# Performance work log

Measured on AMD Instinct MI355X. Metric: run time of the kernel, lower is better.

The kernel has to match this reference:

```python
import jax, jax.numpy as jnp
import numpy as np

T = 8  # number of DP iterations (self.T)

def setup_inputs() -> dict:
    key = jax.random.key(0)
    ks = jax.random.split(key, 9)
    bs, dims, L, d = 16, 4, 2048, 256
    x = jax.random.uniform(ks[0], (bs, dims, L), dtype=jnp.float32)  # one-hot-like input
    s_in = 1.0 / np.sqrt(dims)
    s_d = 1.0 / np.sqrt(d)
    W1 = jax.random.uniform(ks[1], (d, dims), minval=-s_in, maxval=s_in, dtype=jnp.float32)
    b1 = jax.random.uniform(ks[2], (d,), minval=-s_in, maxval=s_in, dtype=jnp.float32)
    W2 = jax.random.uniform(ks[3], (d, d), minval=-s_d, maxval=s_d, dtype=jnp.float32)
    b2 = jax.random.uniform(ks[4], (d,), minval=-s_d, maxval=s_d, dtype=jnp.float32)
    W3 = jax.random.uniform(ks[5], (d, dims), minval=-s_in, maxval=s_in, dtype=jnp.float32)
    b3 = jax.random.uniform(ks[6], (d,), minval=-s_in, maxval=s_in, dtype=jnp.float32)
    W4 = jax.random.uniform(ks[7], (d, d), minval=-s_d, maxval=s_d, dtype=jnp.float32)
    b4 = jax.random.uniform(ks[8], (d,), minval=-s_d, maxval=s_d, dtype=jnp.float32)
    return dict(x=x, W1=W1, b1=b1, W2=W2, b2=b2, W3=W3, b3=b3, W4=W4, b4=b4)

def reference(x, W1, b1, W2, b2, W3, b3, W4, b4):
    # x: (bs, dims, L). The original allocates V:(bs,T+1,L+2,L+2,d) but only the
    # two diagonals V[i,j,j+1] ("up") and V[i,j,j-1] ("down") are ever written/read,
    # so the recurrence collapses to two (bs,L,d) lanes.
    a = jnp.einsum('bdl,od->blo', x, W1) + b1  # W1(x_j) for all j: (bs, L, d)
    bs, L, d = a.shape
    zcol = jnp.zeros((bs, 1, d), a.dtype)
    shift_r = lambda v: jnp.concatenate([zcol, v[:, :-1]], axis=1)  # v[j-1], zero at j=0
    shift_l = lambda v: jnp.concatenate([v[:, 1:], zcol], axis=1)   # v[j+1], zero at j=L-1
    up = jnp.zeros_like(a)   # up[j]   = V[i, j+1, j+2] (0-indexed lane)
    down = jnp.zeros_like(a) # down[j] = V[i, j+1, j]
    for _ in range(T):
        up = jax.nn.relu(a + shift_r(up) @ W2.T + b2)
        down = jax.nn.relu(a + shift_l(down) @ W2.T + b2)
    c = jnp.einsum('bdl,od->blo', x, W3) + b3
    # miu[j] = relu(W3 x_j + W4(V[T,j-1,j]) + W4(V[T,j+1,j]))
    miu = jax.nn.relu(c + (shift_r(up) @ W4.T + b4) + (shift_l(down) @ W4.T + b4))
    return miu  # (bs, L, d)
```

## Files before the change

### kernel.cpp

```cpp
#include <hip/hip_runtime.h>


typedef __bf16 bf16x8 __attribute__((ext_vector_type(8)));
typedef float f32x16 __attribute__((ext_vector_type(16)));

#define MFMA32(a, b, c) __builtin_amdgcn_mfma_f32_32x32x16_bf16(a, b, c, 0, 0, 0)

__device__ __forceinline__ unsigned short f2bf(float f) {
  unsigned int u = __builtin_bit_cast(unsigned int, f);
  u += 0x7fffu + ((u >> 16) & 1u);
  return (unsigned short)(u >> 16);
}
__device__ __forceinline__ float bf2f(unsigned short s) {
  unsigned int u = ((unsigned int)s) << 16;
  return __builtin_bit_cast(float, u);
}

__global__ void prep_kernel(const float* __restrict__ W1, const float* __restrict__ b1,
                            const float* __restrict__ W2, const float* __restrict__ b2,
                            const float* __restrict__ W3, const float* __restrict__ b3,
                            const float* __restrict__ W4, const float* __restrict__ b4,
                            unsigned short* __restrict__ ws) {
  int idx = blockIdx.x * 256 + threadIdx.x;
  if (idx >= 139264) return;
  float v = 0.0f;
  if (idx < 131072) {
    const float* W = (idx < 65536) ? W2 : W4;
    int i = idx & 65535;
    int j = i & 7, f = i >> 3;
    int lane = f & 63, slot = f >> 6;
    int ks = slot & 15, ot = slot >> 4;
    int o = ot * 32 + (lane & 31);
    int k = ks * 16 + (lane >> 5) * 8 + j;
    v = W[o * 256 + k];
  } else {
    int i = idx - 131072;
    bool first = (i < 4096);
    int ii = i & 4095;
    int j = ii & 7, f = ii >> 3;
    int lane = f & 63, ot = f >> 6;
    int o = ot * 32 + (lane & 31);
    if (lane < 32) {
      if (j < 4) v = first ? W1[o * 4 + j] : W3[o * 4 + j];
      else if (j == 4) v = first ? (b1[o] + b2[o]) : (b3[o] + 2.0f * b4[o]);
    }
  }
  ws[idx] = f2bf(v);
}

__global__ __launch_bounds__(256, 2)
void chain_kernel(const float* __restrict__ x, const unsigned short* __restrict__ ws,
                  float* __restrict__ out) {
  __shared__ int4 Ubuf[2][64 * 32];
  __shared__ int4 xw[80];
  __shared__ int4 zc;

  const int tid = threadIdx.x;
  const int l = tid & 63;
  const int w = tid >> 6;
  const int lane31 = l & 31;
  const int khalf = l >> 5;
  const int b = blockIdx.x >> 5;
  const int j0 = (blockIdx.x & 31) * 64;

  const int4* w2f = (const int4*)ws;
  const int4* w4f = (const int4*)(ws + 65536);
  const int4* w1xg = (const int4*)(ws + 131072);
  const int4* w3xg = (const int4*)(ws + 135168);

  if (tid == 0) zc = make_int4(0, 0, 0, 0);
  if (tid < 80) {
    int j = j0 - 8 + tid;
    int4 c = make_int4(0, 0, 0, 0);
    if (j >= 0 && j < 2048) {
      const float* xb = x + (b * 4) * 2048 + j;
      unsigned short h0 = f2bf(xb[0]);
      unsigned short h1 = f2bf(xb[2048]);
      unsigned short h2 = f2bf(xb[4096]);
      unsigned short h3 = f2bf(xb[6144]);
      c = make_int4((int)(h0 | ((unsigned int)h1 << 16)),
                    (int)(h2 | ((unsigned int)h3 << 16)),
                    0x00003f80, 0);
    }
    xw[tid] = c;
  }

  const int ot0 = w * 2;
  bf16x8 w2c[2][8];
  bf16x8 w1x[2];
#pragma unroll
  for (int t2 = 0; t2 < 2; ++t2) {
    w1x[t2] = __builtin_bit_cast(bf16x8, w1xg[(ot0 + t2) * 64 + l]);
#pragma unroll
    for (int ks = 0; ks < 8; ++ks)
      w2c[t2][ks] = __builtin_bit_cast(bf16x8, w2f[((ot0 + t2) * 16 + ks) * 64 + l]);
  }
  __syncthreads();

  const int mrow0 = lane31;
  const int mrow1 = 32 + lane31;

#pragma unroll 1
  for (int phase = 0; phase < 2; ++phase) {
    int4* U = Ubuf[phase];
#pragma unroll 1
    for (int t = 1; t <= 8; ++t) {
      f32x16 acc[2][2] = {};
#pragma unroll
      for (int mt = 0; mt < 2; ++mt) {
        int m = mt ? mrow1 : mrow0;
        int widx = (phase == 0) ? (m + t - 1) : (m + 17 - t);
        const int4* p = (l < 32) ? (xw + widx) : (&zc);
        bf16x8 bx = __builtin_bit_cast(bf16x8, *p);
        acc[mt][0] = MFMA32(w1x[0], bx, acc[mt][0]);
        acc[mt][1] = MFMA32(w1x[1], bx, acc[mt][1]);
      }
      if (t > 1) {
#pragma unroll
        for (int ks = 0; ks < 16; ++ks) {
          int c0 = 2 * ks + khalf;
          bf16x8 bu0 = __builtin_bit_cast(bf16x8, U[mrow0 * 32 + (c0 ^ (mrow0 & 7))]);
          bf16x8 bu1 = __builtin_bit_cast(bf16x8, U[mrow1 * 32 + (c0 ^ (mrow1 & 7))]);
          bf16x8 af0, af1;
          if (ks < 8) { af0 = w2c[0][ks]; af1 = w2c[1][ks]; }
          else {
            af0 = __builtin_bit_cast(bf16x8, w2f[(ot0 * 16 + ks) * 64 + l]);
            af1 = __builtin_bit_cast(bf16x8, w2f[((ot0 + 1) * 16 + ks) * 64 + l]);
          }
          acc[0][0] = MFMA32(af0, bu0, acc[0][0]);
          acc[0][1] = MFMA32(af1, bu0, acc[0][1]);
          acc[1][0] = MFMA32(af0, bu1, acc[1][0]);
          acc[1][1] = MFMA32(af1, bu1, acc[1][1]);
        }
      }
      __syncthreads();
      const bool lastdown = (phase == 1) && (t == 8);
#pragma unroll
      for (int mt = 0; mt < 2; ++mt) {
        int row = mt ? mrow1 : mrow0;
#pragma unroll
        for (int t2 = 0; t2 < 2; ++t2) {
          int ot = ot0 + t2;
#pragma unroll
          for (int q = 0; q < 4; ++q) {
            float v0 = fmaxf(acc[mt][t2][4 * q + 0], 0.0f);
            float v1 = fmaxf(acc[mt][t2][4 * q + 1], 0.0f);
            float v2 = fmaxf(acc[mt][t2][4 * q + 2], 0.0f);
            float v3 = fmaxf(acc[mt][t2][4 * q + 3], 0.0f);
            int co = ot * 4 + q;
            int coff = row * 32 + (co ^ (row & 7));
            if (lastdown) {
              uint2 uv = *(const uint2*)((const char*)(Ubuf[0] + coff) + khalf * 8);
              v0 += bf2f((unsigned short)(uv.x & 0xffffu));
              v1 += bf2f((unsigned short)(uv.x >> 16));
              v2 += bf2f((unsigned short)(uv.y & 0xffffu));
              v3 += bf2f((unsigned short)(uv.y >> 16));
            }
            uint2 pk;
            pk.x = f2bf(v0) | ((unsigned int)f2bf(v1) << 16);
            pk.y = f2bf(v2) | ((unsigned int)f2bf(v3) << 16);
            *(uint2*)((char*)(U + coff) + khalf * 8) = pk;
          }
        }
      }
      __syncthreads();
    }
  }

  {
    f32x16 acc[2][2] = {};
    bf16x8 w3x0 = __builtin_bit_cast(bf16x8, w3xg[ot0 * 64 + l]);
    bf16x8 w3x1 = __builtin_bit_cast(bf16x8, w3xg[(ot0 + 1) * 64 + l]);
#pragma unroll
    for (int mt = 0; mt < 2; ++mt) {
      int m = mt ? mrow1 : mrow0;
      const int4* p = (l < 32) ? (xw + (m + 8)) : (&zc);
      bf16x8 bx = __builtin_bit_cast(bf16x8, *p);
      acc[mt][0] = MFMA32(w3x0, bx, acc[mt][0]);
      acc[mt][1] = MFMA32(w3x1, bx, acc[mt][1]);
    }
    const int4* S = Ubuf[1];
#pragma unroll
    for (int ks = 0; ks < 16; ++ks) {
      int c0 = 2 * ks + khalf;
      bf16x8 bu0 = __builtin_bit_cast(bf16x8, S[mrow0 * 32 + (c0 ^ (mrow0 & 7))]);
      bf16x8 bu1 = __builtin_bit_cast(bf16x8, S[mrow1 * 32 + (c0 ^ (mrow1 & 7))]);
      bf16x8 af0 = __builtin_bit_cast(bf16x8, w4f[(ot0 * 16 + ks) * 64 + l]);
      bf16x8 af1 = __builtin_bit_cast(bf16x8, w4f[((ot0 + 1) * 16 + ks) * 64 + l]);
      acc[0][0] = MFMA32(af0, bu0, acc[0][0]);
      acc[0][1] = MFMA32(af1, bu0, acc[0][1]);
      acc[1][0] = MFMA32(af0, bu1, acc[1][0]);
      acc[1][1] = MFMA32(af1, bu1, acc[1][1]);
    }
#pragma unroll
    for (int mt = 0; mt < 2; ++mt) {
      int m = mt ? mrow1 : mrow0;
      int pbase = (b * 2048 + j0 + m) * 256;
#pragma unroll
      for (int t2 = 0; t2 < 2; ++t2) {
#pragma unroll
        for (int q = 0; q < 4; ++q) {
          int ob = (ot0 + t2) * 32 + 8 * q + 4 * khalf;
          float4 v;
          v.x = fmaxf(acc[mt][t2][4 * q + 0], 0.0f);
          v.y = fmaxf(acc[mt][t2][4 * q + 1], 0.0f);
          v.z = fmaxf(acc[mt][t2][4 * q + 2], 0.0f);
          v.w = fmaxf(acc[mt][t2][4 * q + 3], 0.0f);
          *(float4*)(out + pbase + ob) = v;
        }
      }
    }
  }
}

extern "C" void kernel_launch(void* const* d_in, const int* in_sizes, int n_in,
                              void* d_out, int out_size, void* d_ws, size_t ws_size,
                              hipStream_t stream) {
  const float* x  = (const float*)d_in[0];
  const float* W1 = (const float*)d_in[1];
  const float* b1 = (const float*)d_in[2];
  const float* W2 = (const float*)d_in[3];
  const float* b2 = (const float*)d_in[4];
  const float* W3 = (const float*)d_in[5];
  const float* b3 = (const float*)d_in[6];
  const float* W4 = (const float*)d_in[7];
  const float* b4 = (const float*)d_in[8];
  unsigned short* ws = (unsigned short*)d_ws;

  prep_kernel<<<544, 256, 0, stream>>>(W1, b1, W2, b2, W3, b3, W4, b4, ws);
  chain_kernel<<<512, 256, 0, stream>>>(x, ws, (float*)d_out);
}
```

Baseline: 159.6 us.

## Run up and down recurrence phases concurrently in separate wave groups

Doubles the block to 512 threads so waves 0-3 compute the 'up' recurrence and waves 4-7 the 'down' recurrence at the same time, instead of running the two phases one after the other. The final W4 GEMM is split by row halves across the two wave groups, which accumulate over both U buffers instead of pre-summing them into one. Fewer W2 fragments are cached in registers to fit the 512-thread launch bound. Native bf16 conversions replace the manual packing. The risks are more register pressure and extra global loads of W2.

After: 273.7 us. 71.5% more time.

```diff
diff --git a/kernel.cpp b/kernel.cpp
--- a/kernel.cpp
+++ b/kernel.cpp
@@ -2,6 +2,7 @@
 
 
 typedef __bf16 bf16x8 __attribute__((ext_vector_type(8)));
+typedef __bf16 bf16x4 __attribute__((ext_vector_type(4)));
 typedef float f32x16 __attribute__((ext_vector_type(16)));
 
 #define MFMA32(a, b, c) __builtin_amdgcn_mfma_f32_32x32x16_bf16(a, b, c, 0, 0, 0)
@@ -10,10 +11,6 @@
   unsigned int u = __builtin_bit_cast(unsigned int, f);
   u += 0x7fffu + ((u >> 16) & 1u);
   return (unsigned short)(u >> 16);
-}
-__device__ __forceinline__ float bf2f(unsigned short s) {
-  unsigned int u = ((unsigned int)s) << 16;
-  return __builtin_bit_cast(float, u);
 }
 
 __global__ void prep_kernel(const float* __restrict__ W1, const float* __restrict__ b1,
@@ -48,7 +45,7 @@
   ws[idx] = f2bf(v);
 }
 
-__global__ __launch_bounds__(256, 2)
+__global__ __launch_bounds__(512, 4)
 void chain_kernel(const float* __restrict__ x, const unsigned short* __restrict__ ws,
                   float* __restrict__ out) {
   __shared__ int4 Ubuf[2][64 * 32];
@@ -58,6 +55,8 @@
   const int tid = threadIdx.x;
   const int l = tid & 63;
   const int w = tid >> 6;
+  const int phase = w >> 2;
+  const int ot0 = (w & 3) * 2;
   const int lane31 = l & 31;
   const int khalf = l >> 5;
   const int b = blockIdx.x >> 5;
@@ -85,129 +84,110 @@
     xw[tid] = c;
   }
 
-  const int ot0 = w * 2;
-  bf16x8 w2c[2][8];
+  bf16x8 w2c[2][4];
   bf16x8 w1x[2];
 #pragma unroll
   for (int t2 = 0; t2 < 2; ++t2) {
     w1x[t2] = __builtin_bit_cast(bf16x8, w1xg[(ot0 + t2) * 64 + l]);
 #pragma unroll
-    for (int ks = 0; ks < 8; ++ks)
+    for (int ks = 0; ks < 4; ++ks)
       w2c[t2][ks] = __builtin_bit_cast(bf16x8, w2f[((ot0 + t2) * 16 + ks) * 64 + l]);
   }
   __syncthreads();
 
   const int mrow0 = lane31;
   const int mrow1 = 32 + lane31;
+  int4* U = Ubuf[phase];
 
 #pragma unroll 1
-  for (int phase = 0; phase < 2; ++phase) {
-    int4* U = Ubuf[phase];
-#pragma unroll 1
-    for (int t = 1; t <= 8; ++t) {
-      f32x16 acc[2][2] = {};
-#pragma unroll
-      for (int mt = 0; mt < 2; ++mt) {
-        int m = mt ? mrow1 : mrow0;
-        int widx = (phase == 0) ? (m + t - 1) : (m + 17 - t);
-        const int4* p = (l < 32) ? (xw + widx) : (&zc);
-        bf16x8 bx = __builtin_bit_cast(bf16x8, *p);
-        acc[mt][0] = MFMA32(w1x[0], bx, acc[mt][0]);
-        acc[mt][1] = MFMA32(w1x[1], bx, acc[mt][1]);
-      }
-      if (t > 1) {
-#pragma unroll
-        for (int ks = 0; ks < 16; ++ks) {
-          int c0 = 2 * ks + khalf;
-          bf16x8 bu0 = __builtin_bit_cast(bf16x8, U[mrow0 * 32 + (c0 ^ (mrow0 & 7))]);
-          bf16x8 bu1 = __builtin_bit_cast(bf16x8, U[mrow1 * 32 + (c0 ^ (mrow1 & 7))]);
-          bf16x8 af0, af1;
-          if (ks < 8) { af0 = w2c[0][ks]; af1 = w2c[1][ks]; }
-          else {
-            af0 = __builtin_bit_cast(bf16x8, w2f[(ot0 * 16 + ks) * 64 + l]);
-            af1 = __builtin_bit_cast(bf16x8, w2f[((ot0 + 1) * 16 + ks) * 64 + l]);
-          }
-          acc[0][0] = MFMA32(af0, bu0, acc[0][0]);
-          acc[0][1] = MFMA32(af1, bu0, acc[0][1]);
-          acc[1][0] = MFMA32(af0, bu1, acc[1][0]);
-          acc[1][1] = MFMA32(af1, bu1, acc[1][1]);
+  for (int t = 1; t <= 8; ++t) {
+    f32x16 acc[2][2] = {};
+#pragma unroll
+    for (int mt = 0; mt < 2; ++mt) {
+      int m = mt ? mrow1 : mrow0;
+      int widx = (phase == 0) ? (m + t - 1) : (m + 17 - t);
+      const int4* p = (l < 32) ? (xw + widx) : (&zc);
+      bf16x8 bx = __builtin_bit_cast(bf16x8, *p);
+      acc[mt][0] = MFMA32(w1x[0], bx, acc[mt][0]);
+      acc[mt][1] = MFMA32(w1x[1], bx, acc[mt][1]);
+    }
+    if (t > 1) {
+#pragma unroll
+      for (int ks = 0; ks < 16; ++ks) {
+        int c0 = 2 * ks + khalf;
+        bf16x8 bu0 = __builtin_bit_cast(bf16x8, U[mrow0 * 32 + (c0 ^ (mrow0 & 7))]);
+        bf16x8 bu1 = __builtin_bit_cast(bf16x8, U[mrow1 * 32 + (c0 ^ (mrow1 & 7))]);
+        bf16x8 af0, af1;
+        if (ks < 4) { af0 = w2c[0][ks]; af1 = w2c[1][ks]; }
+        else {
+          af0 = __builtin_bit_cast(bf16x8, w2f[(ot0 * 16 + ks) * 64 + l]);
+          af1 = __builtin_bit_cast(bf16x8, w2f[((ot0 + 1) * 16 + ks) * 64 + l]);
         }
-      }
-      __syncthreads();
-      const bool lastdown = (phase == 1) && (t == 8);
-#pragma unroll
-      for (int mt = 0; mt < 2; ++mt) {
-        int row = mt ? mrow1 : mrow0;
-#pragma unroll
-        for (int t2 = 0; t2 < 2; ++t2) {
-          int ot = ot0 + t2;
-#pragma unroll
-          for (int q = 0; q < 4; ++q) {
-            float v0 = fmaxf(acc[mt][t2][4 * q + 0], 0.0f);
-            float v1 = fmaxf(acc[mt][t2][4 * q + 1], 0.0f);
-            float v2 = fmaxf(acc[mt][t2][4 * q + 2], 0.0f);
-            float v3 = fmaxf(acc[mt][t2][4 * q + 3], 0.0f);
-            int co = ot * 4 + q;
-            int coff = row * 32 + (co ^ (row & 7));
-            if (lastdown) {
-              uint2 uv = *(const uint2*)((const char*)(Ubuf[0] + coff) + khalf * 8);
-              v0 += bf2f((unsigned short)(uv.x & 0xffffu));
-              v1 += bf2f((unsigned short)(uv.x >> 16));
-              v2 += bf2f((unsigned short)(uv.y & 0xffffu));
-              v3 += bf2f((unsigned short)(uv.y >> 16));
-            }
-            uint2 pk;
-            pk.x = f2bf(v0) | ((unsigned int)f2bf(v1) << 16);
-            pk.y = f2bf(v2) | ((unsigned int)f2bf(v3) << 16);
-            *(uint2*)((char*)(U + coff) + khalf * 8) = pk;
-          }
+        acc[0][0] = MFMA32(af0, bu0, acc[0][0]);
+        acc[0][1] = MFMA32(af1, bu0, acc[0][1]);
+        acc[1][0] = MFMA32(af0, bu1, acc[1][0]);
+        acc[1][1] = MFMA32(af1, bu1, acc[1][1]);
+      }
+    }
+    __syncthreads();
+#pragma unroll
+    for (int mt = 0; mt < 2; ++mt) {
+      int row = mt ? mrow1 : mrow0;
+#pragma unroll
+      for (int t2 = 0; t2 < 2; ++t2) {
+        int ot = ot0 + t2;
+#pragma unroll
+        for (int q = 0; q < 4; ++q) {
+          bf16x4 h;
+          h.x = (__bf16)fmaxf(acc[mt][t2][4 * q + 0], 0.0f);
+          h.y = (__bf16)fmaxf(acc[mt][t2][4 * q + 1], 0.0f);
+          h.z = (__bf16)fmaxf(acc[mt][t2][4 * q + 2], 0.0f);
+          h.w = (__bf16)fmaxf(acc[mt][t2][4 * q + 3], 0.0f);
+          int co = ot * 4 + q;
+          int coff = row * 32 + (co ^ (row & 7));
+          *(uint2*)((char*)(U + coff) + khalf * 8) = __builtin_bit_cast(uint2, h);
         }
       }
-      __syncthreads();
-    }
+    }
+    __syncthreads();
   }
 
   {
-    f32x16 acc[2][2] = {};
+    const int mrow = phase * 32 + lane31;
+    f32x16 acc[2] = {};
     bf16x8 w3x0 = __builtin_bit_cast(bf16x8, w3xg[ot0 * 64 + l]);
     bf16x8 w3x1 = __builtin_bit_cast(bf16x8, w3xg[(ot0 + 1) * 64 + l]);
-#pragma unroll
-    for (int mt = 0; mt < 2; ++mt) {
-      int m = mt ? mrow1 : mrow0;
-      const int4* p = (l < 32) ? (xw + (m + 8)) : (&zc);
+    {
+      const int4* p = (l < 32) ? (xw + mrow + 8) : (&zc);
       bf16x8 bx = __builtin_bit_cast(bf16x8, *p);
-      acc[mt][0] = MFMA32(w3x0, bx, acc[mt][0]);
-      acc[mt][1] = MFMA32(w3x1, bx, acc[mt][1]);
-    }
-    const int4* S = Ubuf[1];
-#pragma unroll
-    for (int ks = 0; ks < 16; ++ks) {
-      int c0 = 2 * ks + khalf;
-      bf16x8 bu0 = __builtin_bit_cast(bf16x8, S[mrow0 * 32 + (c0 ^ (mrow0 & 7))]);
-      bf16x8 bu1 = __builtin_bit_cast(bf16x8, S[mrow1 * 32 + (c0 ^ (mrow1 & 7))]);
-      bf16x8 af0 = __builtin_bit_cast(bf16x8, w4f[(ot0 * 16 + ks) * 64 + l]);
-      bf16x8 af1 = __builtin_bit_cast(bf16x8, w4f[((ot0 + 1) * 16 + ks) * 64 + l]);
-      acc[0][0] = MFMA32(af0, bu0, acc[0][0]);
-      acc[0][1] = MFMA32(af1, bu0, acc[0][1]);
-      acc[1][0] = MFMA32(af0, bu1, acc[1][0]);
-      acc[1][1] = MFMA32(af1, bu1, acc[1][1]);
-    }
-#pragma unroll
-    for (int mt = 0; mt < 2; ++mt) {
-      int m = mt ? mrow1 : mrow0;
-      int pbase = (b * 2048 + j0 + m) * 256;
-#pragma unroll
-      for (int t2 = 0; t2 < 2; ++t2) {
-#pragma unroll
-        for (int q = 0; q < 4; ++q) {
-          int ob = (ot0 + t2) * 32 + 8 * q + 4 * khalf;
-          float4 v;
-          v.x = fmaxf(acc[mt][t2][4 * q + 0], 0.0f);
-          v.y = fmaxf(acc[mt][t2][4 * q + 1], 0.0f);
-          v.z = fmaxf(acc[mt][t2][4 * q + 2], 0.0f);
-          v.w = fmaxf(acc[mt][t2][4 * q + 3], 0.0f);
-          *(float4*)(out + pbase + ob) = v;
-        }
+      acc[0] = MFMA32(w3x0, bx, acc[0]);
+      acc[1] = MFMA32(w3x1, bx, acc[1]);
+    }
+#pragma unroll 1
+    for (int ph2 = 0; ph2 < 2; ++ph2) {
+      const int4* S = Ubuf[ph2];
+#pragma unroll
+      for (int ks = 0; ks < 16; ++ks) {
+        int c0 = 2 * ks + khalf;
+        bf16x8 bu = __builtin_bit_cast(bf16x8, S[mrow * 32 + (c0 ^ (mrow & 7))]);
+        bf16x8 af0 = __builtin_bit_cast(bf16x8, w4f[(ot0 * 16 + ks) * 64 + l]);
+        bf16x8 af1 = __builtin_bit_cast(bf16x8, w4f[((ot0 + 1) * 16 + ks) * 64 + l]);
+        acc[0] = MFMA32(af0, bu, acc[0]);
+        acc[1] = MFMA32(af1, bu, acc[1]);
+      }
+    }
+    int pbase = (b * 2048 + j0 + mrow) * 256;
+#pragma unroll
+    for (int t2 = 0; t2 < 2; ++t2) {
+#pragma unroll
+      for (int q = 0; q < 4; ++q) {
+        int ob = (ot0 + t2) * 32 + 8 * q + 4 * khalf;
+        float4 v;
+        v.x = fmaxf(acc[t2][4 * q + 0], 0.0f);
+        v.y = fmaxf(acc[t2][4 * q + 1], 0.0f);
+        v.z = fmaxf(acc[t2][4 * q + 2], 0.0f);
+        v.w = fmaxf(acc[t2][4 * q + 3], 0.0f);
+        *(float4*)(out + pbase + ob) = v;
       }
     }
   }
@@ -228,5 +208,5 @@
   unsigned short* ws = (unsigned short*)d_ws;
 
   prep_kernel<<<544, 256, 0, stream>>>(W1, b1, W2, b2, W3, b3, W4, b4, ws);
-  chain_kernel<<<512, 256, 0, stream>>>(x, ws, (float*)d_out);
-}
+  chain_kernel<<<512, 512, 0, stream>>>(x, ws, (float*)d_out);
+}
```

## Split up/down recurrence phases into separate blocks and add a final W4 kernel

Applied to the files above, without the earlier changes.

The up and down recurrences now run in separate thread blocks (1024 blocks instead of 512), each using a single 32 KB LDS state buffer with a launch bound of 4 blocks per CU. Each block writes its final state to global workspace, and a new final_kernel reloads both states and computes the W3/W4 output. This doubles parallelism and occupancy for the serial 8-step chain. The cost is an extra kernel launch and a global round-trip of the state tiles. The bf16 packing also switches to native __bf16 conversion, and the down state is no longer pre-summed with up before the W4 GEMM; instead two K-passes accumulate, which is more MFMA work in the final stage.

Measured after the change: 254.5 us. +59.5%, slower.

```diff
diff --git a/kernel.cpp b/kernel.cpp
--- a/kernel.cpp
+++ b/kernel.cpp
@@ -2,6 +2,7 @@
 
 
 typedef __bf16 bf16x8 __attribute__((ext_vector_type(8)));
+typedef __bf16 bf16x4 __attribute__((ext_vector_type(4)));
 typedef float f32x16 __attribute__((ext_vector_type(16)));
 
 #define MFMA32(a, b, c) __builtin_amdgcn_mfma_f32_32x32x16_bf16(a, b, c, 0, 0, 0)
@@ -11,10 +12,8 @@
   u += 0x7fffu + ((u >> 16) & 1u);
   return (unsigned short)(u >> 16);
 }
-__device__ __forceinline__ float bf2f(unsigned short s) {
-  unsigned int u = ((unsigned int)s) << 16;
-  return __builtin_bit_cast(float, u);
-}
+
+#define STATE_OFF 139264
 
 __global__ void prep_kernel(const float* __restrict__ W1, const float* __restrict__ b1,
                             const float* __restrict__ W2, const float* __restrict__ b2,
@@ -48,10 +47,9 @@
   ws[idx] = f2bf(v);
 }
 
-__global__ __launch_bounds__(256, 2)
-void chain_kernel(const float* __restrict__ x, const unsigned short* __restrict__ ws,
-                  float* __restrict__ out) {
-  __shared__ int4 Ubuf[2][64 * 32];
+__global__ __launch_bounds__(256, 4)
+void chain_kernel(const float* __restrict__ x, unsigned short* __restrict__ ws) {
+  __shared__ int4 U[64 * 32];
   __shared__ int4 xw[80];
   __shared__ int4 zc;
 
@@ -60,13 +58,13 @@
   const int w = tid >> 6;
   const int lane31 = l & 31;
   const int khalf = l >> 5;
-  const int b = blockIdx.x >> 5;
-  const int j0 = (blockIdx.x & 31) * 64;
+  const int phase = blockIdx.x >> 9;
+  const int tile = blockIdx.x & 511;
+  const int b = tile >> 5;
+  const int j0 = (tile & 31) * 64;
 
   const int4* w2f = (const int4*)ws;
-  const int4* w4f = (const int4*)(ws + 65536);
   const int4* w1xg = (const int4*)(ws + 131072);
-  const int4* w3xg = (const int4*)(ws + 135168);
 
   if (tid == 0) zc = make_int4(0, 0, 0, 0);
   if (tid < 80) {
@@ -101,90 +99,125 @@
   const int mrow1 = 32 + lane31;
 
 #pragma unroll 1
-  for (int phase = 0; phase < 2; ++phase) {
-    int4* U = Ubuf[phase];
-#pragma unroll 1
-    for (int t = 1; t <= 8; ++t) {
-      f32x16 acc[2][2] = {};
-#pragma unroll
-      for (int mt = 0; mt < 2; ++mt) {
-        int m = mt ? mrow1 : mrow0;
-        int widx = (phase == 0) ? (m + t - 1) : (m + 17 - t);
-        const int4* p = (l < 32) ? (xw + widx) : (&zc);
-        bf16x8 bx = __builtin_bit_cast(bf16x8, *p);
-        acc[mt][0] = MFMA32(w1x[0], bx, acc[mt][0]);
-        acc[mt][1] = MFMA32(w1x[1], bx, acc[mt][1]);
+  for (int t = 1; t <= 8; ++t) {
+    f32x16 acc[2][2] = {};
+#pragma unroll
+    for (int mt = 0; mt < 2; ++mt) {
+      int m = mt ? mrow1 : mrow0;
+      int widx = (phase == 0) ? (m + t - 1) : (m + 17 - t);
+      const int4* p = (l < 32) ? (xw + widx) : (&zc);
+      bf16x8 bx = __builtin_bit_cast(bf16x8, *p);
+      acc[mt][0] = MFMA32(w1x[0], bx, acc[mt][0]);
+      acc[mt][1] = MFMA32(w1x[1], bx, acc[mt][1]);
+    }
+    if (t > 1) {
+#pragma unroll
+      for (int ks = 0; ks < 16; ++ks) {
+        int c0 = 2 * ks + khalf;
+        bf16x8 bu0 = __builtin_bit_cast(bf16x8, U[mrow0 * 32 + (c0 ^ (mrow0 & 7))]);
+        bf16x8 bu1 = __builtin_bit_cast(bf16x8, U[mrow1 * 32 + (c0 ^ (mrow1 & 7))]);
+        bf16x8 af0, af1;
+        if (ks < 8) { af0 = w2c[0][ks]; af1 = w2c[1][ks]; }
+        else {
+          af0 = __builtin_bit_cast(bf16x8, w2f[(ot0 * 16 + ks) * 64 + l]);
+          af1 = __builtin_bit_cast(bf16x8, w2f[((ot0 + 1) * 16 + ks) * 64 + l]);
+        }
+        acc[0][0] = MFMA32(af0, bu0, acc[0][0]);
+        acc[0][1] = MFMA32(af1, bu0, acc[0][1]);
+        acc[1][0] = MFMA32(af0, bu1, acc[1][0]);
+        acc[1][1] = MFMA32(af1, bu1, acc[1][1]);
       }
-      if (t > 1) {
-#pragma unroll
-        for (int ks = 0; ks < 16; ++ks) {
-          int c0 = 2 * ks + khalf;
-          bf16x8 bu0 = __builtin_bit_cast(bf16x8, U[mrow0 * 32 + (c0 ^ (mrow0 & 7))]);
-          bf16x8 bu1 = __builtin_bit_cast(bf16x8, U[mrow1 * 32 + (c0 ^ (mrow1 & 7))]);
-          bf16x8 af0, af1;
-          if (ks < 8) { af0 = w2c[0][ks]; af1 = w2c[1][ks]; }
-          else {
-            af0 = __builtin_bit_cast(bf16x8, w2f[(ot0 * 16 + ks) * 64 + l]);
-            af1 = __builtin_bit_cast(bf16x8, w2f[((ot0 + 1) * 16 + ks) * 64 + l]);
-          }
-          acc[0][0] = MFMA32(af0, bu0, acc[0][0]);
-          acc[0][1] = MFMA32(af1, bu0, acc[0][1]);
-          acc[1][0] = MFMA32(af0, bu1, acc[1][0]);
-          acc[1][1] = MFMA32(af1, bu1, acc[1][1]);
+    }
+    __syncthreads();
+#pragma unroll
+    for (int mt = 0; mt < 2; ++mt) {
+      int row = mt ? mrow1 : mrow0;
+#pragma unroll
+      for (int t2 = 0; t2 < 2; ++t2) {
+        int ot = ot0 + t2;
+#pragma unroll
+        for (int q = 0; q < 4; ++q) {
+          bf16x4 h;
+          h.x = (__bf16)fmaxf(acc[mt][t2][4 * q + 0], 0.0f);
+          h.y = (__bf16)fmaxf(acc[mt][t2][4 * q + 1], 0.0f);
+          h.z = (__bf16)fmaxf(acc[mt][t2][4 * q + 2], 0.0f);
+          h.w = (__bf16)fmaxf(acc[mt][t2][4 * q + 3], 0.0f);
+          int co = ot * 4 + q;
+          int coff = row * 32 + (co ^ (row & 7));
+          *(uint2*)((char*)(U + coff) + khalf * 8) = __builtin_bit_cast(uint2, h);
         }
       }
-      __syncthreads();
-      const bool lastdown = (phase == 1) && (t == 8);
-#pragma unroll
-      for (int mt = 0; mt < 2; ++mt) {
-        int row = mt ? mrow1 : mrow0;
-#pragma unroll
-        for (int t2 = 0; t2 < 2; ++t2) {
-          int ot = ot0 + t2;
-#pragma unroll
-          for (int q = 0; q < 4; ++q) {
-            float v0 = fmaxf(acc[mt][t2][4 * q + 0], 0.0f);
-            float v1 = fmaxf(acc[mt][t2][4 * q + 1], 0.0f);
-            float v2 = fmaxf(acc[mt][t2][4 * q + 2], 0.0f);
-            float v3 = fmaxf(acc[mt][t2][4 * q + 3], 0.0f);
-            int co = ot * 4 + q;
-            int coff = row * 32 + (co ^ (row & 7));
-            if (lastdown) {
-              uint2 uv = *(const uint2*)((const char*)(Ubuf[0] + coff) + khalf * 8);
-              v0 += bf2f((unsigned short)(uv.x & 0xffffu));
-              v1 += bf2f((unsigned short)(uv.x >> 16));
-              v2 += bf2f((unsigned short)(uv.y & 0xffffu));
-              v3 += bf2f((unsigned short)(uv.y >> 16));
-            }
-            uint2 pk;
-            pk.x = f2bf(v0) | ((unsigned int)f2bf(v1) << 16);
-            pk.y = f2bf(v2) | ((unsigned int)f2bf(v3) << 16);
-            *(uint2*)((char*)(U + coff) + khalf * 8) = pk;
-          }
-        }
-      }
-      __syncthreads();
-    }
-  }
-
-  {
-    f32x16 acc[2][2] = {};
-    bf16x8 w3x0 = __builtin_bit_cast(bf16x8, w3xg[ot0 * 64 + l]);
-    bf16x8 w3x1 = __builtin_bit_cast(bf16x8, w3xg[(ot0 + 1) * 64 + l]);
-#pragma unroll
-    for (int mt = 0; mt < 2; ++mt) {
-      int m = mt ? mrow1 : mrow0;
-      const int4* p = (l < 32) ? (xw + (m + 8)) : (&zc);
-      bf16x8 bx = __builtin_bit_cast(bf16x8, *p);
-      acc[mt][0] = MFMA32(w3x0, bx, acc[mt][0]);
-      acc[mt][1] = MFMA32(w3x1, bx, acc[mt][1]);
-    }
-    const int4* S = Ubuf[1];
+    }
+    __syncthreads();
+  }
+
+  int4* stg = (int4*)(ws + STATE_OFF) + (phase * 512 + tile) * 2048;
+#pragma unroll
+  for (int i = 0; i < 8; ++i) stg[i * 256 + tid] = U[i * 256 + tid];
+}
+
+__global__ __launch_bounds__(256, 2)
+void final_kernel(const float* __restrict__ x, const unsigned short* __restrict__ ws,
+                  float* __restrict__ out) {
+  __shared__ int4 S[2][64 * 32];
+  __shared__ int4 xw[64];
+  __shared__ int4 zc;
+
+  const int tid = threadIdx.x;
+  const int l = tid & 63;
+  const int w = tid >> 6;
+  const int lane31 = l & 31;
+  const int khalf = l >> 5;
+  const int tile = blockIdx.x;
+  const int b = tile >> 5;
+  const int j0 = (tile & 31) * 64;
+
+  const int4* w4f = (const int4*)(ws + 65536);
+  const int4* w3xg = (const int4*)(ws + 135168);
+  const int4* stg = (const int4*)(ws + STATE_OFF);
+
+  if (tid == 0) zc = make_int4(0, 0, 0, 0);
+  if (tid < 64) {
+    int j = j0 + tid;
+    const float* xb = x + (b * 4) * 2048 + j;
+    unsigned short h0 = f2bf(xb[0]);
+    unsigned short h1 = f2bf(xb[2048]);
+    unsigned short h2 = f2bf(xb[4096]);
+    unsigned short h3 = f2bf(xb[6144]);
+    xw[tid] = make_int4((int)(h0 | ((unsigned int)h1 << 16)),
+                        (int)(h2 | ((unsigned int)h3 << 16)),
+                        0x00003f80, 0);
+  }
+#pragma unroll
+  for (int i = 0; i < 8; ++i) {
+    S[0][i * 256 + tid] = stg[tile * 2048 + i * 256 + tid];
+    S[1][i * 256 + tid] = stg[(512 + tile) * 2048 + i * 256 + tid];
+  }
+  __syncthreads();
+
+  const int ot0 = w * 2;
+  const int mrow0 = lane31;
+  const int mrow1 = 32 + lane31;
+
+  f32x16 acc[2][2] = {};
+  bf16x8 w3x0 = __builtin_bit_cast(bf16x8, w3xg[ot0 * 64 + l]);
+  bf16x8 w3x1 = __builtin_bit_cast(bf16x8, w3xg[(ot0 + 1) * 64 + l]);
+#pragma unroll
+  for (int mt = 0; mt < 2; ++mt) {
+    int m = mt ? mrow1 : mrow0;
+    const int4* p = (l < 32) ? (xw + m) : (&zc);
+    bf16x8 bx = __builtin_bit_cast(bf16x8, *p);
+    acc[mt][0] = MFMA32(w3x0, bx, acc[mt][0]);
+    acc[mt][1] = MFMA32(w3x1, bx, acc[mt][1]);
+  }
+#pragma unroll 1
+  for (int ph = 0; ph < 2; ++ph) {
+    const int4* Sp = S[ph];
 #pragma unroll
     for (int ks = 0; ks < 16; ++ks) {
       int c0 = 2 * ks + khalf;
-      bf16x8 bu0 = __builtin_bit_cast(bf16x8, S[mrow0 * 32 + (c0 ^ (mrow0 & 7))]);
-      bf16x8 bu1 = __builtin_bit_cast(bf16x8, S[mrow1 * 32 + (c0 ^ (mrow1 & 7))]);
+      bf16x8 bu0 = __builtin_bit_cast(bf16x8, Sp[mrow0 * 32 + (c0 ^ (mrow0 & 7))]);
+      bf16x8 bu1 = __builtin_bit_cast(bf16x8, Sp[mrow1 * 32 + (c0 ^ (mrow1 & 7))]);
       bf16x8 af0 = __builtin_bit_cast(bf16x8, w4f[(ot0 * 16 + ks) * 64 + l]);
       bf16x8 af1 = __builtin_bit_cast(bf16x8, w4f[((ot0 + 1) * 16 + ks) * 64 + l]);
       acc[0][0] = MFMA32(af0, bu0, acc[0][0]);
@@ -192,22 +225,22 @@
       acc[1][0] = MFMA32(af0, bu1, acc[1][0]);
       acc[1][1] = MFMA32(af1, bu1, acc[1][1]);
     }
-#pragma unroll
-    for (int mt = 0; mt < 2; ++mt) {
-      int m = mt ? mrow1 : mrow0;
-      int pbase = (b * 2048 + j0 + m) * 256;
-#pragma unroll
-      for (int t2 = 0; t2 < 2; ++t2) {
-#pragma unroll
-        for (int q = 0; q < 4; ++q) {
-          int ob = (ot0 + t2) * 32 + 8 * q + 4 * khalf;
-          float4 v;
-          v.x = fmaxf(acc[mt][t2][4 * q + 0], 0.0f);
-          v.y = fmaxf(acc[mt][t2][4 * q + 1], 0.0f);
-          v.z = fmaxf(acc[mt][t2][4 * q + 2], 0.0f);
-          v.w = fmaxf(acc[mt][t2][4 * q + 3], 0.0f);
-          *(float4*)(out + pbase + ob) = v;
-        }
+  }
+#pragma unroll
+  for (int mt = 0; mt < 2; ++mt) {
+    int m = mt ? mrow1 : mrow0;
+    int pbase = (b * 2048 + j0 + m) * 256;
+#pragma unroll
+    for (int t2 = 0; t2 < 2; ++t2) {
+#pragma unroll
+      for (int q = 0; q < 4; ++q) {
+        int ob = (ot0 + t2) * 32 + 8 * q + 4 * khalf;
+        float4 v;
+        v.x = fmaxf(acc[mt][t2][4 * q + 0], 0.0f);
+        v.y = fmaxf(acc[mt][t2][4 * q + 1], 0.0f);
+        v.z = fmaxf(acc[mt][t2][4 * q + 2], 0.0f);
+        v.w = fmaxf(acc[mt][t2][4 * q + 3], 0.0f);
+        *(float4*)(out + pbase + ob) = v;
       }
     }
   }
@@ -228,5 +261,6 @@
   unsigned short* ws = (unsigned short*)d_ws;
 
   prep_kernel<<<544, 256, 0, stream>>>(W1, b1, W2, b2, W3, b3, W4, b4, ws);
-  chain_kernel<<<512, 256, 0, stream>>>(x, ws, (float*)d_out);
-}
+  chain_kernel<<<1024, 256, 0, stream>>>(x, ws);
+  final_kernel<<<512, 256, 0, stream>>>(x, ws, (float*)d_out);
+}
```

## Interleave up and down recurrences in one loop with column-major LDS layout

Applied to the files above, without the earlier changes.

The two DP chains (up and down) now advance together inside a single 8-step loop, each step issuing MFMAs for both lanes. This halves the number of block barriers and gives the scheduler twice as many independent MFMAs per step to hide latency. The shared buffer moves from a swizzled row layout to a column-major [chunk][row] layout, and the final W4 projection runs separately over both buffers instead of summing them in bf16 first. In exchange the accumulator state doubles (more VGPRs), so the number of register-cached W2 chunks drops from 8 to 6, which adds global reloads.

Result: faster. 135.1 us (-15.4%).

```diff
diff --git a/kernel.cpp b/kernel.cpp
--- a/kernel.cpp
+++ b/kernel.cpp
@@ -2,6 +2,7 @@
 
 
 typedef __bf16 bf16x8 __attribute__((ext_vector_type(8)));
+typedef __bf16 bf16x4 __attribute__((ext_vector_type(4)));
 typedef float f32x16 __attribute__((ext_vector_type(16)));
 
 #define MFMA32(a, b, c) __builtin_amdgcn_mfma_f32_32x32x16_bf16(a, b, c, 0, 0, 0)
@@ -10,10 +11,6 @@
   unsigned int u = __builtin_bit_cast(unsigned int, f);
   u += 0x7fffu + ((u >> 16) & 1u);
   return (unsigned short)(u >> 16);
-}
-__device__ __forceinline__ float bf2f(unsigned short s) {
-  unsigned int u = ((unsigned int)s) << 16;
-  return __builtin_bit_cast(float, u);
 }
 
 __global__ void prep_kernel(const float* __restrict__ W1, const float* __restrict__ b1,
@@ -48,10 +45,12 @@
   ws[idx] = f2bf(v);
 }
 
+#define NC 6
+
 __global__ __launch_bounds__(256, 2)
 void chain_kernel(const float* __restrict__ x, const unsigned short* __restrict__ ws,
                   float* __restrict__ out) {
-  __shared__ int4 Ubuf[2][64 * 32];
+  __shared__ int4 U[2][32 * 64];
   __shared__ int4 xw[80];
   __shared__ int4 zc;
 
@@ -60,8 +59,9 @@
   const int w = tid >> 6;
   const int lane31 = l & 31;
   const int khalf = l >> 5;
-  const int b = blockIdx.x >> 5;
-  const int j0 = (blockIdx.x & 31) * 64;
+  const int tile = blockIdx.x;
+  const int b = tile >> 5;
+  const int j0 = (tile & 31) * 64;
 
   const int4* w2f = (const int4*)ws;
   const int4* w4f = (const int4*)(ws + 65536);
@@ -86,13 +86,13 @@
   }
 
   const int ot0 = w * 2;
-  bf16x8 w2c[2][8];
+  bf16x8 w2c[2][NC];
   bf16x8 w1x[2];
 #pragma unroll
   for (int t2 = 0; t2 < 2; ++t2) {
     w1x[t2] = __builtin_bit_cast(bf16x8, w1xg[(ot0 + t2) * 64 + l]);
 #pragma unroll
-    for (int ks = 0; ks < 8; ++ks)
+    for (int ks = 0; ks < NC; ++ks)
       w2c[t2][ks] = __builtin_bit_cast(bf16x8, w2f[((ot0 + t2) * 16 + ks) * 64 + l]);
   }
   __syncthreads();
@@ -101,40 +101,47 @@
   const int mrow1 = 32 + lane31;
 
 #pragma unroll 1
-  for (int phase = 0; phase < 2; ++phase) {
-    int4* U = Ubuf[phase];
-#pragma unroll 1
-    for (int t = 1; t <= 8; ++t) {
-      f32x16 acc[2][2] = {};
+  for (int t = 1; t <= 8; ++t) {
+    f32x16 acc[2][2][2] = {};
+#pragma unroll
+    for (int ph = 0; ph < 2; ++ph) {
 #pragma unroll
       for (int mt = 0; mt < 2; ++mt) {
         int m = mt ? mrow1 : mrow0;
-        int widx = (phase == 0) ? (m + t - 1) : (m + 17 - t);
+        int widx = (ph == 0) ? (m + t - 1) : (m + 17 - t);
         const int4* p = (l < 32) ? (xw + widx) : (&zc);
         bf16x8 bx = __builtin_bit_cast(bf16x8, *p);
-        acc[mt][0] = MFMA32(w1x[0], bx, acc[mt][0]);
-        acc[mt][1] = MFMA32(w1x[1], bx, acc[mt][1]);
-      }
-      if (t > 1) {
-#pragma unroll
-        for (int ks = 0; ks < 16; ++ks) {
-          int c0 = 2 * ks + khalf;
-          bf16x8 bu0 = __builtin_bit_cast(bf16x8, U[mrow0 * 32 + (c0 ^ (mrow0 & 7))]);
-          bf16x8 bu1 = __builtin_bit_cast(bf16x8, U[mrow1 * 32 + (c0 ^ (mrow1 & 7))]);
-          bf16x8 af0, af1;
-          if (ks < 8) { af0 = w2c[0][ks]; af1 = w2c[1][ks]; }
-          else {
-            af0 = __builtin_bit_cast(bf16x8, w2f[(ot0 * 16 + ks) * 64 + l]);
-            af1 = __builtin_bit_cast(bf16x8, w2f[((ot0 + 1) * 16 + ks) * 64 + l]);
-          }
-          acc[0][0] = MFMA32(af0, bu0, acc[0][0]);
-          acc[0][1] = MFMA32(af1, bu0, acc[0][1]);
-          acc[1][0] = MFMA32(af0, bu1, acc[1][0]);
-          acc[1][1] = MFMA32(af1, bu1, acc[1][1]);
+        acc[ph][mt][0] = MFMA32(w1x[0], bx, acc[ph][mt][0]);
+        acc[ph][mt][1] = MFMA32(w1x[1], bx, acc[ph][mt][1]);
+      }
+    }
+    if (t > 1) {
+#pragma unroll
+      for (int ks = 0; ks < 16; ++ks) {
+        int c0 = 2 * ks + khalf;
+        bf16x8 bu00 = __builtin_bit_cast(bf16x8, U[0][c0 * 64 + mrow0]);
+        bf16x8 bu01 = __builtin_bit_cast(bf16x8, U[0][c0 * 64 + mrow1]);
+        bf16x8 bu10 = __builtin_bit_cast(bf16x8, U[1][c0 * 64 + mrow0]);
+        bf16x8 bu11 = __builtin_bit_cast(bf16x8, U[1][c0 * 64 + mrow1]);
+        bf16x8 af0, af1;
+        if (ks < NC) { af0 = w2c[0][ks]; af1 = w2c[1][ks]; }
+        else {
+          af0 = __builtin_bit_cast(bf16x8, w2f[(ot0 * 16 + ks) * 64 + l]);
+          af1 = __builtin_bit_cast(bf16x8, w2f[((ot0 + 1) * 16 + ks) * 64 + l]);
         }
-      }
-      __syncthreads();
-      const bool lastdown = (phase == 1) && (t == 8);
+        acc[0][0][0] = MFMA32(af0, bu00, acc[0][0][0]);
+        acc[0][0][1] = MFMA32(af1, bu00, acc[0][0][1]);
+        acc[0][1][0] = MFMA32(af0, bu01, acc[0][1][0]);
+        acc[0][1][1] = MFMA32(af1, bu01, acc[0][1][1]);
+        acc[1][0][0] = MFMA32(af0, bu10, acc[1][0][0]);
+        acc[1][0][1] = MFMA32(af1, bu10, acc[1][0][1]);
+        acc[1][1][0] = MFMA32(af0, bu11, acc[1][1][0]);
+        acc[1][1][1] = MFMA32(af1, bu11, acc[1][1][1]);
+      }
+    }
+    __syncthreads();
+#pragma unroll
+    for (int ph = 0; ph < 2; ++ph) {
 #pragma unroll
       for (int mt = 0; mt < 2; ++mt) {
         int row = mt ? mrow1 : mrow0;
@@ -143,28 +150,18 @@
           int ot = ot0 + t2;
 #pragma unroll
           for (int q = 0; q < 4; ++q) {
-            float v0 = fmaxf(acc[mt][t2][4 * q + 0], 0.0f);
-            float v1 = fmaxf(acc[mt][t2][4 * q + 1], 0.0f);
-            float v2 = fmaxf(acc[mt][t2][4 * q + 2], 0.0f);
-            float v3 = fmaxf(acc[mt][t2][4 * q + 3], 0.0f);
-            int co = ot * 4 + q;
-            int coff = row * 32 + (co ^ (row & 7));
-            if (lastdown) {
-              uint2 uv = *(const uint2*)((const char*)(Ubuf[0] + coff) + khalf * 8);
-              v0 += bf2f((unsigned short)(uv.x & 0xffffu));
-              v1 += bf2f((unsigned short)(uv.x >> 16));
-              v2 += bf2f((unsigned short)(uv.y & 0xffffu));
-              v3 += bf2f((unsigned short)(uv.y >> 16));
-            }
-            uint2 pk;
-            pk.x = f2bf(v0) | ((unsigned int)f2bf(v1) << 16);
-            pk.y = f2bf(v2) | ((unsigned int)f2bf(v3) << 16);
-            *(uint2*)((char*)(U + coff) + khalf * 8) = pk;
+            bf16x4 h;
+            h.x = (__bf16)fmaxf(acc[ph][mt][t2][4 * q + 0], 0.0f);
+            h.y = (__bf16)fmaxf(acc[ph][mt][t2][4 * q + 1], 0.0f);
+            h.z = (__bf16)fmaxf(acc[ph][mt][t2][4 * q + 2], 0.0f);
+            h.w = (__bf16)fmaxf(acc[ph][mt][t2][4 * q + 3], 0.0f);
+            int idx = (ot * 4 + q) * 64 + row;
+            *(uint2*)((char*)(U[ph] + idx) + khalf * 8) = __builtin_bit_cast(uint2, h);
           }
         }
       }
-      __syncthreads();
-    }
+    }
+    __syncthreads();
   }
 
   {
@@ -174,23 +171,26 @@
 #pragma unroll
     for (int mt = 0; mt < 2; ++mt) {
       int m = mt ? mrow1 : mrow0;
-      const int4* p = (l < 32) ? (xw + (m + 8)) : (&zc);
+      const int4* p = (l < 32) ? (xw + m + 8) : (&zc);
       bf16x8 bx = __builtin_bit_cast(bf16x8, *p);
       acc[mt][0] = MFMA32(w3x0, bx, acc[mt][0]);
       acc[mt][1] = MFMA32(w3x1, bx, acc[mt][1]);
     }
-    const int4* S = Ubuf[1];
-#pragma unroll
-    for (int ks = 0; ks < 16; ++ks) {
-      int c0 = 2 * ks + khalf;
-      bf16x8 bu0 = __builtin_bit_cast(bf16x8, S[mrow0 * 32 + (c0 ^ (mrow0 & 7))]);
-      bf16x8 bu1 = __builtin_bit_cast(bf16x8, S[mrow1 * 32 + (c0 ^ (mrow1 & 7))]);
-      bf16x8 af0 = __builtin_bit_cast(bf16x8, w4f[(ot0 * 16 + ks) * 64 + l]);
-      bf16x8 af1 = __builtin_bit_cast(bf16x8, w4f[((ot0 + 1) * 16 + ks) * 64 + l]);
-      acc[0][0] = MFMA32(af0, bu0, acc[0][0]);
-      acc[0][1] = MFMA32(af1, bu0, acc[0][1]);
-      acc[1][0] = MFMA32(af0, bu1, acc[1][0]);
-      acc[1][1] = MFMA32(af1, bu1, acc[1][1]);
+#pragma unroll 1
+    for (int ph = 0; ph < 2; ++ph) {
+      const int4* Sp = U[ph];
+#pragma unroll
+      for (int ks = 0; ks < 16; ++ks) {
+        int c0 = 2 * ks + khalf;
+        bf16x8 bu0 = __builtin_bit_cast(bf16x8, Sp[c0 * 64 + mrow0]);
+        bf16x8 bu1 = __builtin_bit_cast(bf16x8, Sp[c0 * 64 + mrow1]);
+        bf16x8 af0 = __builtin_bit_cast(bf16x8, w4f[(ot0 * 16 + ks) * 64 + l]);
+        bf16x8 af1 = __builtin_bit_cast(bf16x8, w4f[((ot0 + 1) * 16 + ks) * 64 + l]);
+        acc[0][0] = MFMA32(af0, bu0, acc[0][0]);
+        acc[0][1] = MFMA32(af1, bu0, acc[0][1]);
+        acc[1][0] = MFMA32(af0, bu1, acc[1][0]);
+        acc[1][1] = MFMA32(af1, bu1, acc[1][1]);
+      }
     }
 #pragma unroll
     for (int mt = 0; mt < 2; ++mt) {
```
